# Kernel tuning notes

Measured on AMD Instinct MI355X. Metric: run time of the kernel, lower is better.

The kernel has to match this reference:

```python
import math
import jax, jax.numpy as jnp
import numpy as np

S, D = 4096, 1024          # cur_seq, input_dim
H, Dh = 8, 64              # head_num, head_dim
ETA, R = 4, 8              # eta, r
E = Dh * ETA               # feature-mapped key dim = eta*head_dim = 256
EPS = 1e-5


def setup_inputs() -> dict:
    key = jax.random.key(0)
    ks = jax.random.split(key, 8)
    inputs = jax.random.normal(ks[0], (S, D), jnp.float32) * 0.1
    terminations = (jax.random.uniform(ks[1], (S,)) < 0.01).astype(jnp.int32)
    W_kqv = jax.random.normal(ks[2], (D, H * Dh * 5), jnp.float32) / np.sqrt(D).astype(np.float32)
    b_kqv = jnp.zeros((H * Dh * 5,), jnp.float32)
    W_p = jax.random.normal(ks[3], (D, H * ETA * 3), jnp.float32) / np.sqrt(D).astype(np.float32)
    b_p = jnp.zeros((H * ETA * 3,), jnp.float32)
    W_proj = jax.random.normal(ks[4], (H * Dh, D), jnp.float32) / np.sqrt(H * Dh).astype(np.float32)
    b_proj = jnp.zeros((D,), jnp.float32)
    tilde_k_prev = jnp.zeros((R, H, E), jnp.float32)
    tilde_v_prev = jnp.zeros((R, H, Dh), jnp.float32)
    s_prev = jnp.zeros((H, E), jnp.float32)
    tick = jnp.ones((1,), jnp.float32)
    return dict(inputs=inputs, terminations=terminations, W_kqv=W_kqv, b_kqv=b_kqv,
                W_p=W_p, b_p=b_p, W_proj=W_proj, b_proj=b_proj,
                tilde_k_prev=tilde_k_prev, tilde_v_prev=tilde_v_prev,
                s_prev=s_prev, tick=tick)


def reference(inputs, terminations, W_kqv, b_kqv, W_p, b_p, W_proj, b_proj,
              tilde_k_prev, tilde_v_prev, s_prev, tick):
    # fused projections
    kqvbg = (inputs @ W_kqv + b_kqv).reshape(S, H, 5, Dh)
    k, q, v, beta, g = (kqvbg[:, :, i] for i in range(5))
    p = (inputs @ W_p + b_p).reshape(S, H, 3, ETA)
    p1, p2, p3 = p[:, :, 0], p[:, :, 1], p[:, :, 2]

    # feature maps: outer product over (Dh, ETA), flattened with Dh outer (matches torch flatten(-2))
    keys = (jax.nn.relu(k)[..., :, None] * jax.nn.relu(p1)[..., None, :]).reshape(S, H, E)
    queries = (jax.nn.relu(q)[..., :, None] * jax.nn.relu(p2)[..., None, :]).reshape(S, H, E)
    gammas = (jax.nn.sigmoid(g)[..., :, None] * jax.nn.sigmoid(p3)[..., None, :]).reshape(S, H, E)
    beta = jax.nn.sigmoid(beta)  # (S,H,Dh)

    # oscillation basis
    ticks = tick[0] + jnp.arange(1, S + 1, dtype=inputs.dtype)       # (S,)
    omegas = jnp.linspace(-math.pi, math.pi, R).astype(inputs.dtype)  # (R,)
    occil = jnp.cos(ticks[:, None] * omegas[None, :])                 # (S,R)

    vals = v * beta                                                   # (S,H,Dh)
    vals_r = vals[:, None] * occil[:, :, None, None]                  # (S,R,H,Dh)
    keys_g = keys * gammas                                            # (S,H,E)
    s_seq = keys_g
    keys_r = keys_g[:, None] * occil[:, :, None, None]                # (S,R,H,E)

    nt = (1.0 - terminations.astype(inputs.dtype))[:, None, None]
    dg = (1.0 - gammas) * nt                                          # (S,H,E)
    db = (1.0 - beta) * nt                                            # (S,H,Dh)

    def step(carry, xs):
        kc, vc, sc = carry
        kt, vt, st, dgt, dbt = xs
        kc = dgt[None] * kc + kt   # (R,H,E)
        vc = dbt[None] * vc + vt   # (R,H,Dh)
        sc = dgt * sc + st         # (H,E)
        return (kc, vc, sc), (kc, vc, sc)

    _, (fk, fv, fs) = jax.lax.scan(step, (tilde_k_prev, tilde_v_prev, s_prev),
                                   (keys_r, vals_r, s_seq, dg, db))

    kdq = jnp.einsum('srhe,she->srh', fk, queries)
    kv = jnp.einsum('srhd,srh->shd', fv, kdq)
    norm = jnp.einsum('she,she->sh', fs, queries)
    attn = kv / (2.0 * R * norm[..., None] + EPS)                     # (S,H,Dh)
    out = attn.reshape(S, H * Dh) @ W_proj + b_proj                   # (S,D)
    return out
```

## Files before the change

### kernel.cpp

```cpp
#include <hip/hip_runtime.h>
#include <hip/hip_bf16.h>

#define S_    4096
#define D_    1024
#define H_    8
#define DH_   64
#define ETA_  4
#define R_    8
#define E_    256
#define NC_   256
#define LC_   (S_/NC_)
#define N1_   2688
#define NKQV_ 2560
#define NP_   96
#define PIF   3.14159265358979323846

#define PB_CVT    2048
#define PB_TRWK   (PB_CVT + 640)
#define PB_TRWP   (PB_TRWK + 32)
#define PB_TRWPJ  (PB_TRWP + 128)
#define PB_OC     (PB_TRWPJ + 128)
#define PB_BIAS   (PB_OC + 11)
#define PB_TOTAL  PB_BIAS

typedef unsigned short u16;
typedef unsigned int   u32;
typedef _Float16 v8h __attribute__((ext_vector_type(8)));
typedef float v4f __attribute__((ext_vector_type(4)));

__device__ __forceinline__ u16 f2h(float f) {
    _Float16 h = (_Float16)f;
    return __builtin_bit_cast(unsigned short, h);
}
__device__ __forceinline__ float h2f(u16 u) {
    return (float)__builtin_bit_cast(_Float16, u);
}
__device__ __forceinline__ float sigm(float x) { return 1.f / (1.f + expf(-x)); }

#define GLD16(gp, lp) __builtin_amdgcn_global_load_lds( \
    (const __attribute__((address_space(1))) u32*)(const void*)(gp), \
    (__attribute__((address_space(3))) u32*)(void*)(lp), 16, 0, 0)

__device__ __forceinline__ void tr64h(float (*tile)[65], const float* __restrict__ src, int K, int Nsrc,
                                      u16* __restrict__ dH, int rowOff, int k0, int n0, int t) {
    const int cc = t & 63, rr = t >> 6;
    #pragma unroll
    for (int i = 0; i < 16; ++i) {
        int kk = rr * 16 + i;
        tile[kk][cc] = (n0 + cc < Nsrc) ? src[(size_t)(k0 + kk) * Nsrc + n0 + cc] : 0.f;
    }
    __syncthreads();
    #pragma unroll
    for (int i = 0; i < 16; ++i) {
        int nn = rr * 16 + i;
        dH[(size_t)(rowOff + n0 + nn) * K + k0 + cc] = f2h(tile[cc][nn]);
    }
}

__global__ __launch_bounds__(256) void prep_all(const float* __restrict__ inputs,
                                                const float* __restrict__ Wk, const float* __restrict__ Wp,
                                                const float* __restrict__ Wproj,
                                                const float* __restrict__ bk, const float* __restrict__ bp,
                                                const float* __restrict__ tick,
                                                u16* __restrict__ AbfH, u16* __restrict__ AbfL,
                                                u16* __restrict__ BTh, u16* __restrict__ WpTh,
                                                float* __restrict__ biasb, float* __restrict__ OC) {
    __shared__ float tile[64][65];
    const int b = blockIdx.x, t = threadIdx.x;
    if (b < PB_CVT) {
        int i = b * 256 + t;
        const float4* xp = (const float4*)inputs;
        float4 a = xp[2 * i], bb = xp[2 * i + 1];
        float v[8] = {a.x, a.y, a.z, a.w, bb.x, bb.y, bb.z, bb.w};
        unsigned hh[8], ll[8];
        #pragma unroll
        for (int j = 0; j < 8; ++j) {
            u16 h = f2h(v[j]);
            hh[j] = h;
            ll[j] = f2h(v[j] - h2f(h));
        }
        uint4 rh, rl;
        rh.x = hh[0] | (hh[1] << 16); rh.y = hh[2] | (hh[3] << 16);
        rh.z = hh[4] | (hh[5] << 16); rh.w = hh[6] | (hh[7] << 16);
        rl.x = ll[0] | (ll[1] << 16); rl.y = ll[2] | (ll[3] << 16);
        rl.z = ll[4] | (ll[5] << 16); rl.w = ll[6] | (ll[7] << 16);
        ((uint4*)AbfH)[i] = rh;
        ((uint4*)AbfL)[i] = rl;
    } else if (b < PB_TRWK) {
        int i = b - PB_CVT;
        tr64h(tile, Wk, D_, NKQV_, BTh, 0, (i % 16) * 64, (i / 16) * 64, t);
    } else if (b < PB_TRWP) {
        int i = b - PB_TRWK;
        tr64h(tile, Wp, D_, NP_, BTh, NKQV_, (i % 16) * 64, (i / 16) * 64, t);
    } else if (b < PB_TRWPJ) {
        int i = b - PB_TRWP;
        tr64h(tile, Wproj, 512, D_, WpTh, 0, (i % 8) * 64, (i / 8) * 64, t);
    } else if (b < PB_OC) {
        int idx = (b - PB_TRWPJ) * 256 + t;
        int tt = idx / R_, r = idx % R_;
        float start = (float)(-PIF), stop = (float)PIF;
        float step = __fdiv_rn(__fsub_rn(stop, start), 7.0f);
        float om = __fadd_rn(start, __fmul_rn((float)r, step));
        float tk = __fadd_rn(tick[0], (float)(tt + 1));
        OC[idx] = cosf(__fmul_rn(tk, om));
    } else {
        int n = (b - PB_OC) * 256 + t;
        if (n < N1_)
            biasb[n] = n < NKQV_ ? bk[n] : (n < NKQV_ + NP_ ? bp[n - NKQV_] : 0.f);
    }
}

__global__ __launch_bounds__(256, 3) void gemm_x2_pipe(const u16* __restrict__ Ah, const u16* __restrict__ Al,
                                                       const u16* __restrict__ BTh,
                                                       const float* __restrict__ bias,
                                                       float* __restrict__ Yo, int ldy, int Kdim, int actMode) {
    __shared__ __align__(16) u16 lds[2][3][4096];
    const int tid = threadIdx.x, lane = tid & 63, w = tid >> 6;
    const int mw = (w >> 1) * 64, nw = (w & 1) * 64;
    const int l15 = lane & 15, lk8 = lane >> 4;
    const int lke = (lk8 ^ (l15 & 3) ^ ((l15 >> 2) & 3)) * 8;
    const int gx = gridDim.x;
    const int nb = gx * gridDim.y;
    const int orig = blockIdx.y * gx + blockIdx.x;
    const int per = nb >> 3;
    const int swz = (orig & 7) * per + (orig >> 3);
    const int m0 = (swz / gx) * 128, n0 = (swz % gx) * 128;
    const int nk = Kdim >> 5;

    auto stage = [&](int buf, int k0) {
        #pragma unroll
        for (int c = 0; c < 2; ++c) {
            int u = tid + (c << 8);
            int row = u >> 2, s = u & 3;
            int kc = ((s ^ (row & 3) ^ ((row >> 2) & 3)) << 3);
            int wub = ((u & ~63) << 3);
            size_t offA = (size_t)(m0 + row) * Kdim + k0 + kc;
            size_t offB = (size_t)(n0 + row) * Kdim + k0 + kc;
            GLD16(Ah  + offA, &lds[buf][0][wub]);
            GLD16(Al  + offA, &lds[buf][1][wub]);
            GLD16(BTh + offB, &lds[buf][2][wub]);
        }
    };

    v4f acc[4][4] = {};
    stage(0, 0);
    int cur = 0;
    for (int kt = 0; kt < nk; ++kt) {
        __syncthreads();
        if (kt + 1 < nk) stage(cur ^ 1, (kt + 1) << 5);
        v8h afh[4], afl[4], bfh[4];
        #pragma unroll
        for (int f = 0; f < 4; ++f) {
            int ra = (mw + f * 16 + l15) * 32 + lke;
            int rb = (nw + f * 16 + l15) * 32 + lke;
            afh[f] = *(const v8h*)&lds[cur][0][ra];
            afl[f] = *(const v8h*)&lds[cur][1][ra];
            bfh[f] = *(const v8h*)&lds[cur][2][rb];
        }
        #pragma unroll
        for (int i = 0; i < 4; ++i)
            #pragma unroll
            for (int j = 0; j < 4; ++j) {
                acc[i][j] = __builtin_amdgcn_mfma_f32_16x16x32_f16(afh[i], bfh[j], acc[i][j], 0, 0, 0);
                acc[i][j] = __builtin_amdgcn_mfma_f32_16x16x32_f16(afl[i], bfh[j], acc[i][j], 0, 0, 0);
            }
        cur ^= 1;
    }
    #pragma unroll
    for (int i = 0; i < 4; ++i) {
        int row0 = m0 + mw + i * 16 + lk8 * 4;
        #pragma unroll
        for (int j = 0; j < 4; ++j) {
            int col = n0 + nw + j * 16 + l15;
            float bv = bias[col];
            int ct = 2;
            if (actMode) {
                if (col < NKQV_) ct = (col % 320) >> 6;
                else { int m12 = (col - NKQV_) % 12; ct = (m12 < 8) ? 0 : 3; }
            }
            #pragma unroll
            for (int rg = 0; rg < 4; ++rg) {
                float y = acc[i][j][rg] + bv;
                if (ct == 0 || ct == 1) y = fmaxf(y, 0.f);
                else if (ct >= 3) y = sigm(y);
                Yo[(size_t)(row0 + rg) * ldy + col] = y;
            }
        }
    }
}

__global__ __launch_bounds__(64) void scan_p1(const float* __restrict__ Y1, const float* __restrict__ OC,
                                              const int* __restrict__ term, float* __restrict__ CL) {
    const int b = blockIdx.x, c = b / H_, h = b % H_, lane = threadIdx.x;
    float kc[R_][ETA_] = {}, vc[R_] = {}, sc[ETA_] = {};
    float Pg[ETA_] = {1.f, 1.f, 1.f, 1.f}, Pb = 1.f;
    for (int t = c * LC_; t < c * LC_ + LC_; ++t) {
        const float* row = Y1 + (size_t)t * N1_;
        const float* bh = row + h * 320;
        float rk = bh[lane], vv = bh[128 + lane], sb = bh[192 + lane], sg = bh[256 + lane];
        const float* pp = row + NKQV_ + h * 12;
        float nt = 1.f - (float)term[t];
        float vals = vv * sb, dbv = (1.f - sb) * nt;
        float occ[R_];
        #pragma unroll
        for (int r = 0; r < R_; ++r) occ[r] = OC[t * R_ + r];
        #pragma unroll
        for (int e = 0; e < ETA_; ++e) {
            float gam = sg * pp[8 + e];
            float kg = rk * pp[e] * gam;
            float dgv = (1.f - gam) * nt;
            sc[e] = dgv * sc[e] + kg;
            Pg[e] *= dgv;
            #pragma unroll
            for (int r = 0; r < R_; ++r) kc[r][e] = dgv * kc[r][e] + kg * occ[r];
        }
        Pb *= dbv;
        #pragma unroll
        for (int r = 0; r < R_; ++r) vc[r] = dbv * vc[r] + vals * occ[r];
    }
    float* out = CL + (size_t)b * 49 * 64;
    #pragma unroll
    for (int r = 0; r < R_; ++r)
        #pragma unroll
        for (int e = 0; e < ETA_; ++e) out[(r * 4 + e) * 64 + lane] = kc[r][e];
    #pragma unroll
    for (int r = 0; r < R_; ++r) out[(32 + r) * 64 + lane] = vc[r];
    #pragma unroll
    for (int e = 0; e < ETA_; ++e) out[(40 + e) * 64 + lane] = sc[e];
    #pragma unroll
    for (int e = 0; e < ETA_; ++e) out[(44 + e) * 64 + lane] = Pg[e];
    out[48 * 64 + lane] = Pb;
}

__global__ __launch_bounds__(64) void scan_comb(const float* __restrict__ CL, float* __restrict__ CI,
                                                const float* __restrict__ TK, const float* __restrict__ TV,
                                                const float* __restrict__ SP) {
    const int gid = blockIdx.x * 64 + threadIdx.x;
    const int lane = gid & 63;
    const int hv = gid >> 6;
    const int h = hv / 44;
    const int v = hv % 44;
    float x;
    int dvec;
    if (v < 32) {
        int r = v >> 2, e = v & 3;
        x = TK[((size_t)r * H_ + h) * E_ + lane * 4 + e];
        dvec = 44 + e;
    } else if (v < 40) {
        int r = v - 32;
        x = TV[((size_t)r * H_ + h) * DH_ + lane];
        dvec = 48;
    } else {
        int e = v - 40;
        x = SP[(size_t)h * E_ + lane * 4 + e];
        dvec = 44 + e;
    }
    const float* clb = CL + (size_t)h * 49 * 64 + (size_t)v * 64 + lane;
    const float* dcb = CL + (size_t)h * 49 * 64 + (size_t)dvec * 64 + lane;
    float* cib = CI + (size_t)h * 44 * 64 + (size_t)v * 64 + lane;
    const size_t sCL = (size_t)H_ * 49 * 64;
    const size_t sCI = (size_t)H_ * 44 * 64;
    #pragma unroll 8
    for (int c = 0; c < NC_; ++c) {
        cib[(size_t)c * sCI] = x;
        float cl = clb[(size_t)c * sCL];
        float d  = dcb[(size_t)c * sCL];
        x = fmaf(d, x, cl);
    }
}

__global__ __launch_bounds__(64) void scan_p3(const float* __restrict__ Y1, const float* __restrict__ OC,
                                              const int* __restrict__ term, const float* __restrict__ CI,
                                              u16* __restrict__ attnH, u16* __restrict__ attnL) {
    const int b = blockIdx.x, c = b / H_, h = b % H_, lane = threadIdx.x;
    float kc[R_][ETA_], vc[R_], sc[ETA_];
    const float* ci = CI + (size_t)b * 44 * 64;
    #pragma unroll
    for (int r = 0; r < R_; ++r)
        #pragma unroll
        for (int e = 0; e < ETA_; ++e) kc[r][e] = ci[(r * 4 + e) * 64 + lane];
    #pragma unroll
    for (int r = 0; r < R_; ++r) vc[r] = ci[(32 + r) * 64 + lane];
    #pragma unroll
    for (int e = 0; e < ETA_; ++e) sc[e] = ci[(40 + e) * 64 + lane];
    for (int t = c * LC_; t < c * LC_ + LC_; ++t) {
        const float* row = Y1 + (size_t)t * N1_;
        const float* bh = row + h * 320;
        float rk = bh[lane], rq = bh[64 + lane], vv = bh[128 + lane], sb = bh[192 + lane], sg = bh[256 + lane];
        const float* pp = row + NKQV_ + h * 12;
        float nt = 1.f - (float)term[t];
        float vals = vv * sb, dbv = (1.f - sb) * nt;
        float occ[R_];
        #pragma unroll
        for (int r = 0; r < R_; ++r) occ[r] = OC[t * R_ + r];
        float qe[ETA_];
        #pragma unroll
        for (int e = 0; e < ETA_; ++e) {
            float gam = sg * pp[8 + e];
            float kg = rk * pp[e] * gam;
            float dgv = (1.f - gam) * nt;
            qe[e] = rq * pp[4 + e];
            sc[e] = dgv * sc[e] + kg;
            #pragma unroll
            for (int r = 0; r < R_; ++r) kc[r][e] = dgv * kc[r][e] + kg * occ[r];
        }
        #pragma unroll
        for (int r = 0; r < R_; ++r) vc[r] = dbv * vc[r] + vals * occ[r];
        float kdq[R_], nrm = 0.f;
        #pragma unroll
        for (int r = 0; r < R_; ++r) {
            float s = 0.f;
            #pragma unroll
            for (int e = 0; e < ETA_; ++e) s += kc[r][e] * qe[e];
            kdq[r] = s;
        }
        #pragma unroll
        for (int e = 0; e < ETA_; ++e) nrm += sc[e] * qe[e];
        #pragma unroll
        for (int m = 1; m < 64; m <<= 1) {
            #pragma unroll
            for (int r = 0; r < R_; ++r) kdq[r] += __shfl_xor(kdq[r], m);
            nrm += __shfl_xor(nrm, m);
        }
        float kv = 0.f;
        #pragma unroll
        for (int r = 0; r < R_; ++r) kv += vc[r] * kdq[r];
        float at = kv / (2.f * R_ * nrm + 1e-5f);
        size_t oi = (size_t)t * (H_ * DH_) + h * DH_ + lane;
        u16 hi = f2h(at);
        attnH[oi] = hi;
        attnL[oi] = f2h(at - h2f(hi));
    }
}

extern "C" void kernel_launch(void* const* d_in, const int* in_sizes, int n_in,
                              void* d_out, int out_size, void* d_ws, size_t ws_size,
                              hipStream_t stream) {
    const float* inputs = (const float*)d_in[0];
    const int*   term   = (const int*)d_in[1];
    const float* Wk     = (const float*)d_in[2];
    const float* bk     = (const float*)d_in[3];
    const float* Wp     = (const float*)d_in[4];
    const float* bp     = (const float*)d_in[5];
    const float* Wproj  = (const float*)d_in[6];
    const float* bproj  = (const float*)d_in[7];
    const float* TK     = (const float*)d_in[8];
    const float* TV     = (const float*)d_in[9];
    const float* SP     = (const float*)d_in[10];
    const float* tick   = (const float*)d_in[11];
    float* out = (float*)d_out;

    char* w = (char*)d_ws;
    u16* AbfH   = (u16*)w;  w += (size_t)S_ * D_ * 2;
    u16* AbfL   = (u16*)w;  w += (size_t)S_ * D_ * 2;
    u16* BTh    = (u16*)w;  w += (size_t)N1_ * D_ * 2;
    u16* WpTh   = (u16*)w;  w += (size_t)D_ * 512 * 2;
    u16* attnH  = (u16*)w;  w += (size_t)S_ * 512 * 2;
    u16* attnL  = (u16*)w;  w += (size_t)S_ * 512 * 2;
    float* biasb = (float*)w; w += (size_t)N1_ * 4;
    float* Y1   = (float*)w; w += (size_t)S_ * N1_ * 4;
    float* OC   = (float*)w; w += (size_t)S_ * R_ * 4;
    float* CL   = (float*)w; w += (size_t)NC_ * H_ * 49 * 64 * 4;
    float* CI   = (float*)w; w += (size_t)NC_ * H_ * 44 * 64 * 4;

    prep_all<<<PB_TOTAL, 256, 0, stream>>>(inputs, Wk, Wp, Wproj, bk, bp, tick,
                                           AbfH, AbfL, BTh, WpTh, biasb, OC);
    gemm_x2_pipe<<<dim3(N1_ / 128, S_ / 128), 256, 0, stream>>>(AbfH, AbfL, BTh, biasb, Y1, N1_, D_, 1);
    scan_p1<<<NC_ * H_, 64, 0, stream>>>(Y1, OC, term, CL);
    scan_comb<<<(H_ * 44 * 64) / 64, 64, 0, stream>>>(CL, CI, TK, TV, SP);
    scan_p3<<<NC_ * H_, 64, 0, stream>>>(Y1, OC, term, CI, attnH, attnL);
    gemm_x2_pipe<<<dim3(1024 / 128, S_ / 128), 256, 0, stream>>>(attnH, attnL, WpTh, bproj, out, D_, 512, 0);
}
```

Baseline: 160.3 us.

## Load GEMM MFMA fragments directly from global memory instead of LDS staging

Replaces the double-buffered LDS staging in the split-fp16 GEMM with direct per-lane global vector loads of the A-high, A-low and B fragments for each MFMA. The goal is to drop the LDS traffic and the per-iteration block barrier. The price is that data shared across waves is no longer reused through LDS, so each wave refetches its A and B rows from global memory or cache. The loads are also less coalesced, since each lane reads 16 bytes from a different row.

```diff
diff --git a/kernel.cpp b/kernel.cpp
--- a/kernel.cpp
+++ b/kernel.cpp
@@ -36,10 +36,6 @@
     return (float)__builtin_bit_cast(_Float16, u);
 }
 __device__ __forceinline__ float sigm(float x) { return 1.f / (1.f + expf(-x)); }
-
-#define GLD16(gp, lp) __builtin_amdgcn_global_load_lds( \
-    (const __attribute__((address_space(1))) u32*)(const void*)(gp), \
-    (__attribute__((address_space(3))) u32*)(void*)(lp), 16, 0, 0)
 
 __device__ __forceinline__ void tr64h(float (*tile)[65], const float* __restrict__ src, int K, int Nsrc,
                                       u16* __restrict__ dH, int rowOff, int k0, int n0, int t) {
@@ -110,15 +106,13 @@
     }
 }
 
-__global__ __launch_bounds__(256, 3) void gemm_x2_pipe(const u16* __restrict__ Ah, const u16* __restrict__ Al,
-                                                       const u16* __restrict__ BTh,
-                                                       const float* __restrict__ bias,
-                                                       float* __restrict__ Yo, int ldy, int Kdim, int actMode) {
-    __shared__ __align__(16) u16 lds[2][3][4096];
+__global__ __launch_bounds__(256, 3) void gemm_x2_reg(const u16* __restrict__ Ah, const u16* __restrict__ Al,
+                                                      const u16* __restrict__ BTh,
+                                                      const float* __restrict__ bias,
+                                                      float* __restrict__ Yo, int ldy, int Kdim, int actMode) {
     const int tid = threadIdx.x, lane = tid & 63, w = tid >> 6;
     const int mw = (w >> 1) * 64, nw = (w & 1) * 64;
     const int l15 = lane & 15, lk8 = lane >> 4;
-    const int lke = (lk8 ^ (l15 & 3) ^ ((l15 >> 2) & 3)) * 8;
     const int gx = gridDim.x;
     const int nb = gx * gridDim.y;
     const int orig = blockIdx.y * gx + blockIdx.x;
@@ -127,44 +121,35 @@
     const int m0 = (swz / gx) * 128, n0 = (swz % gx) * 128;
     const int nk = Kdim >> 5;
 
-    auto stage = [&](int buf, int k0) {
-        #pragma unroll
-        for (int c = 0; c < 2; ++c) {
-            int u = tid + (c << 8);
-            int row = u >> 2, s = u & 3;
-            int kc = ((s ^ (row & 3) ^ ((row >> 2) & 3)) << 3);
-            int wub = ((u & ~63) << 3);
-            size_t offA = (size_t)(m0 + row) * Kdim + k0 + kc;
-            size_t offB = (size_t)(n0 + row) * Kdim + k0 + kc;
-            GLD16(Ah  + offA, &lds[buf][0][wub]);
-            GLD16(Al  + offA, &lds[buf][1][wub]);
-            GLD16(BTh + offB, &lds[buf][2][wub]);
-        }
-    };
+    size_t aOff[4], bOff[4];
+    #pragma unroll
+    for (int f = 0; f < 4; ++f) {
+        aOff[f] = (size_t)(m0 + mw + f * 16 + l15) * Kdim + lk8 * 8;
+        bOff[f] = (size_t)(n0 + nw + f * 16 + l15) * Kdim + lk8 * 8;
+    }
 
     v4f acc[4][4] = {};
-    stage(0, 0);
-    int cur = 0;
+    #pragma unroll 2
     for (int kt = 0; kt < nk; ++kt) {
-        __syncthreads();
-        if (kt + 1 < nk) stage(cur ^ 1, (kt + 1) << 5);
-        v8h afh[4], afl[4], bfh[4];
+        const int ko = kt << 5;
+        v8h afh[4], bfh[4], afl[4];
         #pragma unroll
         for (int f = 0; f < 4; ++f) {
-            int ra = (mw + f * 16 + l15) * 32 + lke;
-            int rb = (nw + f * 16 + l15) * 32 + lke;
-            afh[f] = *(const v8h*)&lds[cur][0][ra];
-            afl[f] = *(const v8h*)&lds[cur][1][ra];
-            bfh[f] = *(const v8h*)&lds[cur][2][rb];
-        }
+            afh[f] = *(const v8h*)(Ah + aOff[f] + ko);
+            bfh[f] = *(const v8h*)(BTh + bOff[f] + ko);
+        }
+        #pragma unroll
+        for (int f = 0; f < 4; ++f) afl[f] = *(const v8h*)(Al + aOff[f] + ko);
         #pragma unroll
         for (int i = 0; i < 4; ++i)
             #pragma unroll
-            for (int j = 0; j < 4; ++j) {
+            for (int j = 0; j < 4; ++j)
                 acc[i][j] = __builtin_amdgcn_mfma_f32_16x16x32_f16(afh[i], bfh[j], acc[i][j], 0, 0, 0);
+        #pragma unroll
+        for (int i = 0; i < 4; ++i)
+            #pragma unroll
+            for (int j = 0; j < 4; ++j)
                 acc[i][j] = __builtin_amdgcn_mfma_f32_16x16x32_f16(afl[i], bfh[j], acc[i][j], 0, 0, 0);
-            }
-        cur ^= 1;
     }
     #pragma unroll
     for (int i = 0; i < 4; ++i) {
@@ -365,9 +350,9 @@
 
     prep_all<<<PB_TOTAL, 256, 0, stream>>>(inputs, Wk, Wp, Wproj, bk, bp, tick,
                                            AbfH, AbfL, BTh, WpTh, biasb, OC);
-    gemm_x2_pipe<<<dim3(N1_ / 128, S_ / 128), 256, 0, stream>>>(AbfH, AbfL, BTh, biasb, Y1, N1_, D_, 1);
+    gemm_x2_reg<<<dim3(N1_ / 128, S_ / 128), 256, 0, stream>>>(AbfH, AbfL, BTh, biasb, Y1, N1_, D_, 1);
     scan_p1<<<NC_ * H_, 64, 0, stream>>>(Y1, OC, term, CL);
     scan_comb<<<(H_ * 44 * 64) / 64, 64, 0, stream>>>(CL, CI, TK, TV, SP);
     scan_p3<<<NC_ * H_, 64, 0, stream>>>(Y1, OC, term, CI, attnH, attnL);
-    gemm_x2_pipe<<<dim3(1024 / 128, S_ / 128), 256, 0, stream>>>(attnH, attnL, WpTh, bproj, out, D_, 512, 0);
-}
+    gemm_x2_reg<<<dim3(1024 / 128, S_ / 128), 256, 0, stream>>>(attnH, attnL, WpTh, bproj, out, D_, 512, 0);
+}
```

After: 269.8 us. 1.68x slower.

## Pre-tile weights into MFMA fragment layout and load B directly to registers

Applied to the files above, without the earlier changes.

The weight transpose now writes B in a fragment-native tiled layout (16 rows by 32 k per 512-element block), so each lane can load its MFMA B operand straight from global memory into registers. LDS staging for B is removed, which cuts shared memory per block and LDS read traffic, and the next k-tile's B is prefetched into registers. The MFMA loops are also reordered so all hi-part products run before the lo-part products. The cost is more register pressure and exposed global latency on B, which relies on L2 reuse across blocks.

```diff
diff --git a/kernel.cpp b/kernel.cpp
--- a/kernel.cpp
+++ b/kernel.cpp
@@ -41,9 +41,11 @@
     (const __attribute__((address_space(1))) u32*)(const void*)(gp), \
     (__attribute__((address_space(3))) u32*)(void*)(lp), 16, 0, 0)
 
+
 __device__ __forceinline__ void tr64h(float (*tile)[65], const float* __restrict__ src, int K, int Nsrc,
                                       u16* __restrict__ dH, int rowOff, int k0, int n0, int t) {
     const int cc = t & 63, rr = t >> 6;
+    const int nkt = K >> 5;
     #pragma unroll
     for (int i = 0; i < 16; ++i) {
         int kk = rr * 16 + i;
@@ -53,7 +55,10 @@
     #pragma unroll
     for (int i = 0; i < 16; ++i) {
         int nn = rr * 16 + i;
-        dH[(size_t)(rowOff + n0 + nn) * K + k0 + cc] = f2h(tile[cc][nn]);
+        int nrow = rowOff + n0 + nn, k = k0 + cc;
+        int nt = nrow >> 4, kt = k >> 5;
+        int ln = (nrow & 15) + (((k & 31) >> 3) << 4), j = k & 7;
+        dH[((size_t)(nt * nkt + kt) << 9) + ln * 8 + j] = f2h(tile[cc][nn]);
     }
 }
 
@@ -110,11 +115,11 @@
     }
 }
 
-__global__ __launch_bounds__(256, 3) void gemm_x2_pipe(const u16* __restrict__ Ah, const u16* __restrict__ Al,
-                                                       const u16* __restrict__ BTh,
-                                                       const float* __restrict__ bias,
-                                                       float* __restrict__ Yo, int ldy, int Kdim, int actMode) {
-    __shared__ __align__(16) u16 lds[2][3][4096];
+__global__ __launch_bounds__(256, 3) void gemm_x2_hyb(const u16* __restrict__ Ah, const u16* __restrict__ Al,
+                                                      const u16* __restrict__ BTf,
+                                                      const float* __restrict__ bias,
+                                                      float* __restrict__ Yo, int ldy, int Kdim, int actMode) {
+    __shared__ __align__(16) u16 lds[2][2][4096];
     const int tid = threadIdx.x, lane = tid & 63, w = tid >> 6;
     const int mw = (w >> 1) * 64, nw = (w & 1) * 64;
     const int l15 = lane & 15, lk8 = lane >> 4;
@@ -125,9 +130,9 @@
     const int per = nb >> 3;
     const int swz = (orig & 7) * per + (orig >> 3);
     const int m0 = (swz / gx) * 128, n0 = (swz % gx) * 128;
-    const int nk = Kdim >> 5;
-
-    auto stage = [&](int buf, int k0) {
+    const int nkt = Kdim >> 5;
+
+    auto stageA = [&](int buf, int k0) {
         #pragma unroll
         for (int c = 0; c < 2; ++c) {
             int u = tid + (c << 8);
@@ -135,35 +140,52 @@
             int kc = ((s ^ (row & 3) ^ ((row >> 2) & 3)) << 3);
             int wub = ((u & ~63) << 3);
             size_t offA = (size_t)(m0 + row) * Kdim + k0 + kc;
-            size_t offB = (size_t)(n0 + row) * Kdim + k0 + kc;
-            GLD16(Ah  + offA, &lds[buf][0][wub]);
-            GLD16(Al  + offA, &lds[buf][1][wub]);
-            GLD16(BTh + offB, &lds[buf][2][wub]);
+            GLD16(Ah + offA, &lds[buf][0][wub]);
+            GLD16(Al + offA, &lds[buf][1][wub]);
         }
     };
 
+    size_t bBase[4];
+    #pragma unroll
+    for (int f = 0; f < 4; ++f)
+        bBase[f] = ((size_t)(((n0 + nw) >> 4) + f) * nkt << 9) + lane * 8;
+
     v4f acc[4][4] = {};
-    stage(0, 0);
+    stageA(0, 0);
+    v8h bcur[4];
+    #pragma unroll
+    for (int f = 0; f < 4; ++f) bcur[f] = *(const v8h*)(BTf + bBase[f]);
     int cur = 0;
-    for (int kt = 0; kt < nk; ++kt) {
+    for (int kt = 0; kt < nkt; ++kt) {
         __syncthreads();
-        if (kt + 1 < nk) stage(cur ^ 1, (kt + 1) << 5);
-        v8h afh[4], afl[4], bfh[4];
+        if (kt + 1 < nkt) stageA(cur ^ 1, (kt + 1) << 5);
+        v8h bnxt[4];
+        if (kt + 1 < nkt) {
+            const size_t ko = (size_t)(kt + 1) << 9;
+            #pragma unroll
+            for (int f = 0; f < 4; ++f) bnxt[f] = *(const v8h*)(BTf + bBase[f] + ko);
+        }
+        v8h afh[4], afl[4];
         #pragma unroll
         for (int f = 0; f < 4; ++f) {
             int ra = (mw + f * 16 + l15) * 32 + lke;
-            int rb = (nw + f * 16 + l15) * 32 + lke;
             afh[f] = *(const v8h*)&lds[cur][0][ra];
             afl[f] = *(const v8h*)&lds[cur][1][ra];
-            bfh[f] = *(const v8h*)&lds[cur][2][rb];
         }
         #pragma unroll
         for (int i = 0; i < 4; ++i)
             #pragma unroll
-            for (int j = 0; j < 4; ++j) {
-                acc[i][j] = __builtin_amdgcn_mfma_f32_16x16x32_f16(afh[i], bfh[j], acc[i][j], 0, 0, 0);
-                acc[i][j] = __builtin_amdgcn_mfma_f32_16x16x32_f16(afl[i], bfh[j], acc[i][j], 0, 0, 0);
-            }
+            for (int j = 0; j < 4; ++j)
+                acc[i][j] = __builtin_amdgcn_mfma_f32_16x16x32_f16(afh[i], bcur[j], acc[i][j], 0, 0, 0);
+        #pragma unroll
+        for (int i = 0; i < 4; ++i)
+            #pragma unroll
+            for (int j = 0; j < 4; ++j)
+                acc[i][j] = __builtin_amdgcn_mfma_f32_16x16x32_f16(afl[i], bcur[j], acc[i][j], 0, 0, 0);
+        if (kt + 1 < nkt) {
+            #pragma unroll
+            for (int f = 0; f < 4; ++f) bcur[f] = bnxt[f];
+        }
         cur ^= 1;
     }
     #pragma unroll
@@ -365,9 +387,9 @@
 
     prep_all<<<PB_TOTAL, 256, 0, stream>>>(inputs, Wk, Wp, Wproj, bk, bp, tick,
                                            AbfH, AbfL, BTh, WpTh, biasb, OC);
-    gemm_x2_pipe<<<dim3(N1_ / 128, S_ / 128), 256, 0, stream>>>(AbfH, AbfL, BTh, biasb, Y1, N1_, D_, 1);
+    gemm_x2_hyb<<<dim3(N1_ / 128, S_ / 128), 256, 0, stream>>>(AbfH, AbfL, BTh, biasb, Y1, N1_, D_, 1);
     scan_p1<<<NC_ * H_, 64, 0, stream>>>(Y1, OC, term, CL);
     scan_comb<<<(H_ * 44 * 64) / 64, 64, 0, stream>>>(CL, CI, TK, TV, SP);
     scan_p3<<<NC_ * H_, 64, 0, stream>>>(Y1, OC, term, CI, attnH, attnL);
-    gemm_x2_pipe<<<dim3(1024 / 128, S_ / 128), 256, 0, stream>>>(attnH, attnL, WpTh, bproj, out, D_, 512, 0);
-}
+    gemm_x2_hyb<<<dim3(1024 / 128, S_ / 128), 256, 0, stream>>>(attnH, attnL, WpTh, bproj, out, D_, 512, 0);
+}
```

Measured after the change: 161.6 us. About the same (+0.8%).
